# Kernel optimization log

Measured on AMD Instinct MI355X. Metric: run time of the kernel, lower is better.

## Reference

```python
import jax, jax.numpy as jnp
import numpy as np

TEMPERATURE = 0.07
B, D, NUM_CLASSES = 8192, 256, 100

def setup_inputs() -> dict:
    key = jax.random.key(0)
    kz, kl = jax.random.split(key)
    z = jax.random.normal(kz, (B, D), dtype=jnp.float32)
    z = z / jnp.linalg.norm(z, axis=-1, keepdims=True)  # unit-norm embeddings keep exp(logits/T) finite
    labels = jax.random.randint(kl, (B,), 0, NUM_CLASSES, dtype=jnp.int64)
    return {"z": z, "labels": labels}

def reference(z, labels):
    n = z.shape[0]
    same = labels[:, None] == labels[None, :]              # [B, B] bool
    eye = jnp.eye(n, dtype=bool)
    pos_mask = (same & ~eye).astype(z.dtype)               # positives exclude self
    neg_mask = (~same).astype(z.dtype)                     # mask == 0 entries
    exp_logits = jnp.exp(z @ z.T / TEMPERATURE)            # [B, B]
    sum_neg = jnp.sum(exp_logits * neg_mask, axis=1)       # [B]
    # per positive pair: -log(e_ij / (e_ij + sum_neg_i))
    pair_loss = jnp.log1p(sum_neg[:, None] / exp_logits)   # = -log(e/(e+sn)), stable form
    pos_cnt = jnp.sum(pos_mask, axis=1)                    # [B]
    row_loss = jnp.sum(pair_loss * pos_mask, axis=1) / jnp.maximum(pos_cnt, 1.0)
    valid = (pos_cnt > 0).astype(z.dtype)
    n_valid = jnp.sum(valid)
    loss = jnp.where(n_valid > 0,
                     jnp.sum(row_loss * valid) / jnp.maximum(n_valid, 1.0),
                     jnp.zeros((), z.dtype))
    return loss
```

## Files before the change

kernel.cpp:

```cpp
#include <hip/hip_runtime.h>
#include <hip/hip_bf16.h>


#define BN 8192
#define DD 256
#define INV_T (1.0f / 0.07f)
#define CAPI 256
#define CAP 160
#define IPAD 164

typedef __attribute__((ext_vector_type(8))) __bf16 bf16x8;
typedef __attribute__((ext_vector_type(4))) float f32x4;

static __device__ __forceinline__ unsigned short f2bf(float f) {
    unsigned int u = __builtin_bit_cast(unsigned int, f);
    u = (u + 0x7FFFu + ((u >> 16) & 1u)) >> 16;
    return (unsigned short)u;
}
static __device__ __forceinline__ float bf2f(unsigned short s) {
    unsigned int u = (unsigned int)s << 16;
    return __builtin_bit_cast(float, u);
}

__global__ __launch_bounds__(256) void k_prep(const float* __restrict__ z,
                                              unsigned short* __restrict__ zbf2,
                                              const int* __restrict__ labels,
                                              int* __restrict__ cls_cnt,
                                              int* __restrict__ cls_idx) {
    const int gid = blockIdx.x * 256 + threadIdx.x;
    const float4* z4 = (const float4*)z;
    float4 v0 = z4[gid * 2 + 0];
    float4 v1 = z4[gid * 2 + 1];
    unsigned short r[8];
    r[0] = f2bf(v0.x); r[1] = f2bf(v0.y); r[2] = f2bf(v0.z); r[3] = f2bf(v0.w);
    r[4] = f2bf(v1.x); r[5] = f2bf(v1.y); r[6] = f2bf(v1.z); r[7] = f2bf(v1.w);
    const int j = gid >> 5, c5 = gid & 31;
    const int idx16 = (((j >> 4) * 8 + (c5 >> 2)) * 64) + (c5 & 3) * 16 + (j & 15);
    ((uint4*)zbf2)[idx16] = *(const uint4*)r;
    if (gid < BN) {
        const int c = labels[gid];
        const int slot = atomicAdd(&cls_cnt[c], 1);
        if (slot < CAPI) cls_idx[c * CAPI + slot] = gid;
    }
}

__global__ __launch_bounds__(512, 2) void k_passA(const char* __restrict__ zb2,
                                                  float* __restrict__ sn_part) {
    __shared__ float sn_lds[64];
    const int tid = threadIdx.x;
    const int w = tid >> 6, lane = tid & 63;
    const int l15 = lane & 15, lk = lane >> 4;
    const int rowbase = (blockIdx.x >> 2) * 64;
    const int cq = blockIdx.x & 3;
    const int jt0 = cq * 128 + w * 16;

    if (tid < 64) sn_lds[tid] = 0.f;
    __syncthreads();

    const int rt0 = rowbase >> 4;
    bf16x8 a[4][8];
#pragma unroll
    for (int m = 0; m < 4; ++m) {
        const char* p = zb2 + ((size_t)(rt0 + m) * 8192) + lane * 16;
#pragma unroll
        for (int kf = 0; kf < 8; ++kf)
            a[m][kf] = *(const bf16x8*)(p + kf * 1024);
    }

    float snp[4][4] = {};
    bf16x8 b0[8], b1[8];

    auto loadB = [&](bf16x8 (&dst)[8], int jt) {
        const char* p = zb2 + ((size_t)jt * 8192) + lane * 16;
#pragma unroll
        for (int kf = 0; kf < 8; ++kf)
            dst[kf] = *(const bf16x8*)(p + kf * 1024);
    };
    auto computeTile = [&](bf16x8 (&bx)[8], int jt) {
        f32x4 acc[4] = {};
        __builtin_amdgcn_s_setprio(1);
#pragma unroll
        for (int kf = 0; kf < 8; ++kf)
#pragma unroll
            for (int m = 0; m < 4; ++m)
                acc[m] = __builtin_amdgcn_mfma_f32_16x16x32_bf16(a[m][kf], bx[kf], acc[m], 0, 0, 0);
        __builtin_amdgcn_s_setprio(0);
        const int jj = jt * 16 + l15;
#pragma unroll
        for (int m = 0; m < 4; ++m) {
            const int ig = rowbase + m * 16 + lk * 4;
#pragma unroll
            for (int rr = 0; rr < 4; ++rr) {
                float e = __expf(acc[m][rr] * INV_T);
                if (ig + rr == jj) e = 0.f;
                snp[m][rr] += e;
            }
        }
    };

    loadB(b0, jt0);
    for (int t = 0; t < 16; t += 2) {
        loadB(b1, jt0 + t + 1);
        computeTile(b0, jt0 + t);
        if (t + 2 < 16) loadB(b0, jt0 + t + 2);
        computeTile(b1, jt0 + t + 1);
    }

#pragma unroll
    for (int m = 0; m < 4; ++m) {
#pragma unroll
        for (int rr = 0; rr < 4; ++rr) {
            float v = snp[m][rr];
            v += __shfl_xor(v, 1, 64);
            v += __shfl_xor(v, 2, 64);
            v += __shfl_xor(v, 4, 64);
            v += __shfl_xor(v, 8, 64);
            if (l15 == 0)
                atomicAdd(&sn_lds[m * 16 + lk * 4 + rr], v);
        }
    }
    __syncthreads();
    if (tid < 64)
        sn_part[(size_t)cq * BN + rowbase + tid] = sn_lds[tid];
}

__global__ __launch_bounds__(512) void k_passB(const float* __restrict__ zf,
                                               const float* __restrict__ sn_part,
                                               const int* __restrict__ cls_cnt,
                                               const int* __restrict__ cls_idx,
                                               float* __restrict__ gacc) {
    __shared__ char Zc[CAP * 512];
    __shared__ unsigned short dmat[CAP * IPAD];
    __shared__ int glist[CAP];
    __shared__ float snl[CAP];
    __shared__ float sums[CAP];
    __shared__ float blkL;

    const int c = blockIdx.x;
    const int tid = threadIdx.x;
    const int w = tid >> 6, lane = tid & 63;
    const int l15 = lane & 15, lk = lane >> 4;

    const int n_c = min(cls_cnt[c], CAP);
    const int nt = (n_c + 15) >> 4;
    const int rows_p = nt * 16;

    if (tid < CAP) glist[tid] = (tid < n_c) ? cls_idx[c * CAPI + tid] : 0;
    if (tid == 0) blkL = 0.f;
    __syncthreads();

    for (int e2 = w * 2; e2 < rows_p; e2 += 16) {
        const int row = e2 + (lane >> 5);
        const int li = lane & 31;
        const float* src = zf + (size_t)glist[row] * DD + li * 8;
        float4 v0 = *(const float4*)(src);
        float4 v1 = *(const float4*)(src + 4);
        unsigned short r[8];
        r[0] = f2bf(v0.x); r[1] = f2bf(v0.y); r[2] = f2bf(v0.z); r[3] = f2bf(v0.w);
        r[4] = f2bf(v1.x); r[5] = f2bf(v1.y); r[6] = f2bf(v1.z); r[7] = f2bf(v1.w);
        *(uint4*)(Zc + row * 512 + ((li * 16) ^ ((row & 7) << 4))) = *(const uint4*)r;
    }
    __syncthreads();

    for (int mi = w; mi < nt; mi += 8) {
        const int rowA = mi * 16 + l15;
        const int swa = (rowA & 7) << 4;
        bf16x8 a[8];
#pragma unroll
        for (int kf = 0; kf < 8; ++kf)
            a[kf] = *(const bf16x8*)(Zc + rowA * 512 + ((lk * 16 + kf * 64) ^ swa));
        float sp[4] = {};
        for (int nj = 0; nj < nt; ++nj) {
            const int colB = nj * 16 + l15;
            const int swb = (colB & 7) << 4;
            bf16x8 b[8];
#pragma unroll
            for (int kf = 0; kf < 8; ++kf)
                b[kf] = *(const bf16x8*)(Zc + colB * 512 + ((lk * 16 + kf * 64) ^ swb));
            f32x4 acc = {};
#pragma unroll
            for (int kf = 0; kf < 8; ++kf)
                acc = __builtin_amdgcn_mfma_f32_16x16x32_bf16(a[kf], b[kf], acc, 0, 0, 0);
            unsigned short ep[4];
#pragma unroll
            for (int rr = 0; rr < 4; ++rr) {
                const int i = mi * 16 + lk * 4 + rr;
                const float e = __expf(acc[rr] * INV_T);
                ep[rr] = f2bf(e);
                sp[rr] += (colB < n_c && i != colB) ? e : 0.f;
            }
            uint2 uv;
            uv.x = (unsigned)ep[0] | ((unsigned)ep[1] << 16);
            uv.y = (unsigned)ep[2] | ((unsigned)ep[3] << 16);
            *(uint2*)&dmat[colB * IPAD + mi * 16 + lk * 4] = uv;
        }
#pragma unroll
        for (int rr = 0; rr < 4; ++rr) {
            float v = sp[rr];
            v += __shfl_xor(v, 1, 64);
            v += __shfl_xor(v, 2, 64);
            v += __shfl_xor(v, 4, 64);
            v += __shfl_xor(v, 8, 64);
            if (l15 == 0) sums[mi * 16 + lk * 4 + rr] = v;
        }
    }
    __syncthreads();
    if (tid < CAP)
        snl[tid] = (tid < n_c)
            ? (sn_part[glist[tid]] + sn_part[BN + glist[tid]]
               + sn_part[2 * BN + glist[tid]] + sn_part[3 * BN + glist[tid]]
               - sums[tid])
            : 0.f;
    __syncthreads();

    for (int mi = w; mi < nt; mi += 8) {
        float sneg[4];
#pragma unroll
        for (int rr = 0; rr < 4; ++rr) {
            const int i = mi * 16 + lk * 4 + rr;
            sneg[rr] = (i < n_c) ? snl[i] : 0.f;
        }
        float sp[4] = {};
        for (int nj = 0; nj < nt; ++nj) {
            const int colB = nj * 16 + l15;
            const uint2 pk = *(const uint2*)&dmat[colB * IPAD + mi * 16 + lk * 4];
            float ev[4];
            ev[0] = bf2f((unsigned short)(pk.x & 0xffff));
            ev[1] = bf2f((unsigned short)(pk.x >> 16));
            ev[2] = bf2f((unsigned short)(pk.y & 0xffff));
            ev[3] = bf2f((unsigned short)(pk.y >> 16));
#pragma unroll
            for (int rr = 0; rr < 4; ++rr) {
                const int i = mi * 16 + lk * 4 + rr;
                const float t = log1pf(sneg[rr] / ev[rr]);
                sp[rr] += (colB < n_c && i != colB) ? t : 0.f;
            }
        }
#pragma unroll
        for (int rr = 0; rr < 4; ++rr) {
            float v = sp[rr];
            v += __shfl_xor(v, 1, 64);
            v += __shfl_xor(v, 2, 64);
            v += __shfl_xor(v, 4, 64);
            v += __shfl_xor(v, 8, 64);
            const int i = mi * 16 + lk * 4 + rr;
            if (l15 == 0 && i < n_c && n_c > 1)
                atomicAdd(&blkL, v / (float)(n_c - 1));
        }
    }
    __syncthreads();
    if (tid == 0 && n_c > 1) {
        atomicAdd(&gacc[0], blkL);
        atomicAdd(&gacc[1], (float)n_c);
    }
}

__global__ void k_final(const float* __restrict__ gacc, float* __restrict__ out) {
    if (threadIdx.x == 0) {
        const float L = gacc[0], V = gacc[1];
        out[0] = (V > 0.f) ? L / fmaxf(V, 1.f) : 0.f;
    }
}

extern "C" void kernel_launch(void* const* d_in, const int* in_sizes, int n_in,
                              void* d_out, int out_size, void* d_ws, size_t ws_size,
                              hipStream_t stream) {
    const float* z      = (const float*)d_in[0];
    const int*   labels = (const int*)d_in[1];
    float* out = (float*)d_out;

    char* ws = (char*)d_ws;
    unsigned short* zbf2 = (unsigned short*)ws;
    size_t off = (size_t)BN * DD * sizeof(unsigned short);
    float* sn_part = (float*)(ws + off);  off += 4 * BN * sizeof(float);
    int*   cls_cnt = (int*)(ws + off);    off += 1024;
    float* gacc    = (float*)(ws + off);  off += 8;
    int*   cls_idx = (int*)(ws + off);    off += 100 * CAPI * sizeof(int);

    hipMemsetAsync(cls_cnt, 0, 1032, stream);
    k_prep  <<<1024, 256, 0, stream>>>(z, zbf2, labels, cls_cnt, cls_idx);
    k_passA <<<512, 512, 0, stream>>>((const char*)zbf2, sn_part);
    k_passB <<<100, 512, 0, stream>>>(z, sn_part, cls_cnt, cls_idx, gacc);
    k_final <<<1, 64, 0, stream>>>(gacc, out);
}
```

Before: 87.74 us.

## Retile negative-sum pass, drop diagonal masking, split class pass across two blocks

The negative-sum pass now uses 256-thread blocks. Each wave owns 8 row tiles (128 rows) over a 16-column-tile chunk, which raises A-fragment reuse and cuts B loads per MFMA. Per-row sums go straight into one global array through atomics, replacing the LDS reduction and the 4-way partial buffer. The diagonal masks are removed from both passes because the self term cancels when the in-class sum is subtracted. The class pass is launched with a second grid dimension so each class's row tiles are split across two blocks, doubling parallelism at the cost of loading the class embeddings twice. The larger register footprint (64 A fragments plus accumulators) risks spills or lower occupancy.

```diff
diff --git a/kernel.cpp b/kernel.cpp
--- a/kernel.cpp
+++ b/kernel.cpp
@@ -44,30 +44,27 @@
     }
 }
 
-__global__ __launch_bounds__(512, 2) void k_passA(const char* __restrict__ zb2,
-                                                  float* __restrict__ sn_part) {
-    __shared__ float sn_lds[64];
+__global__ __launch_bounds__(256, 2) void k_passA(const char* __restrict__ zb2,
+                                                  float* __restrict__ sn) {
     const int tid = threadIdx.x;
     const int w = tid >> 6, lane = tid & 63;
     const int l15 = lane & 15, lk = lane >> 4;
-    const int rowbase = (blockIdx.x >> 2) * 64;
-    const int cq = blockIdx.x & 3;
-    const int jt0 = cq * 128 + w * 16;
-
-    if (tid < 64) sn_lds[tid] = 0.f;
-    __syncthreads();
-
-    const int rt0 = rowbase >> 4;
-    bf16x8 a[4][8];
-#pragma unroll
-    for (int m = 0; m < 4; ++m) {
+    const int rowblk = blockIdx.x >> 5;
+    const int cchunk = blockIdx.x & 31;
+    const int rowwave = rowblk * 512 + w * 128;
+    const int jt0 = cchunk * 16;
+
+    const int rt0 = rowwave >> 4;
+    bf16x8 a[8][8];
+#pragma unroll
+    for (int m = 0; m < 8; ++m) {
         const char* p = zb2 + ((size_t)(rt0 + m) * 8192) + lane * 16;
 #pragma unroll
         for (int kf = 0; kf < 8; ++kf)
             a[m][kf] = *(const bf16x8*)(p + kf * 1024);
     }
 
-    float snp[4][4] = {};
+    float snp[8][4] = {};
     bf16x8 b0[8], b1[8];
 
     auto loadB = [&](bf16x8 (&dst)[8], int jt) {
@@ -76,38 +73,32 @@
         for (int kf = 0; kf < 8; ++kf)
             dst[kf] = *(const bf16x8*)(p + kf * 1024);
     };
-    auto computeTile = [&](bf16x8 (&bx)[8], int jt) {
-        f32x4 acc[4] = {};
-        __builtin_amdgcn_s_setprio(1);
-#pragma unroll
-        for (int kf = 0; kf < 8; ++kf)
-#pragma unroll
-            for (int m = 0; m < 4; ++m)
+    auto computeTile = [&](bf16x8 (&bx)[8]) {
+        f32x4 acc[8];
+#pragma unroll
+        for (int m = 0; m < 8; ++m) acc[m] = (f32x4){0.f, 0.f, 0.f, 0.f};
+#pragma unroll
+        for (int kf = 0; kf < 8; ++kf)
+#pragma unroll
+            for (int m = 0; m < 8; ++m)
                 acc[m] = __builtin_amdgcn_mfma_f32_16x16x32_bf16(a[m][kf], bx[kf], acc[m], 0, 0, 0);
-        __builtin_amdgcn_s_setprio(0);
-        const int jj = jt * 16 + l15;
-#pragma unroll
-        for (int m = 0; m < 4; ++m) {
-            const int ig = rowbase + m * 16 + lk * 4;
-#pragma unroll
-            for (int rr = 0; rr < 4; ++rr) {
-                float e = __expf(acc[m][rr] * INV_T);
-                if (ig + rr == jj) e = 0.f;
-                snp[m][rr] += e;
-            }
-        }
+#pragma unroll
+        for (int m = 0; m < 8; ++m)
+#pragma unroll
+            for (int rr = 0; rr < 4; ++rr)
+                snp[m][rr] += __expf(acc[m][rr] * INV_T);
     };
 
     loadB(b0, jt0);
     for (int t = 0; t < 16; t += 2) {
         loadB(b1, jt0 + t + 1);
-        computeTile(b0, jt0 + t);
+        computeTile(b0);
         if (t + 2 < 16) loadB(b0, jt0 + t + 2);
-        computeTile(b1, jt0 + t + 1);
-    }
-
-#pragma unroll
-    for (int m = 0; m < 4; ++m) {
+        computeTile(b1);
+    }
+
+#pragma unroll
+    for (int m = 0; m < 8; ++m) {
 #pragma unroll
         for (int rr = 0; rr < 4; ++rr) {
             float v = snp[m][rr];
@@ -116,16 +107,13 @@
             v += __shfl_xor(v, 4, 64);
             v += __shfl_xor(v, 8, 64);
             if (l15 == 0)
-                atomicAdd(&sn_lds[m * 16 + lk * 4 + rr], v);
-        }
-    }
-    __syncthreads();
-    if (tid < 64)
-        sn_part[(size_t)cq * BN + rowbase + tid] = sn_lds[tid];
+                atomicAdd(&sn[rowwave + m * 16 + lk * 4 + rr], v);
+        }
+    }
 }
 
 __global__ __launch_bounds__(512) void k_passB(const float* __restrict__ zf,
-                                               const float* __restrict__ sn_part,
+                                               const float* __restrict__ sn,
                                                const int* __restrict__ cls_cnt,
                                                const int* __restrict__ cls_idx,
                                                float* __restrict__ gacc) {
@@ -137,6 +125,7 @@
     __shared__ float blkL;
 
     const int c = blockIdx.x;
+    const int y = blockIdx.y;
     const int tid = threadIdx.x;
     const int w = tid >> 6, lane = tid & 63;
     const int l15 = lane & 15, lk = lane >> 4;
@@ -162,7 +151,7 @@
     }
     __syncthreads();
 
-    for (int mi = w; mi < nt; mi += 8) {
+    for (int mi = 2 * w + y; mi < nt; mi += 16) {
         const int rowA = mi * 16 + l15;
         const int swa = (rowA & 7) << 4;
         bf16x8 a[8];
@@ -184,10 +173,9 @@
             unsigned short ep[4];
 #pragma unroll
             for (int rr = 0; rr < 4; ++rr) {
-                const int i = mi * 16 + lk * 4 + rr;
                 const float e = __expf(acc[rr] * INV_T);
                 ep[rr] = f2bf(e);
-                sp[rr] += (colB < n_c && i != colB) ? e : 0.f;
+                sp[rr] += (colB < n_c) ? e : 0.f;
             }
             uint2 uv;
             uv.x = (unsigned)ep[0] | ((unsigned)ep[1] << 16);
@@ -206,14 +194,10 @@
     }
     __syncthreads();
     if (tid < CAP)
-        snl[tid] = (tid < n_c)
-            ? (sn_part[glist[tid]] + sn_part[BN + glist[tid]]
-               + sn_part[2 * BN + glist[tid]] + sn_part[3 * BN + glist[tid]]
-               - sums[tid])
-            : 0.f;
-    __syncthreads();
-
-    for (int mi = w; mi < nt; mi += 8) {
+        snl[tid] = (tid < n_c) ? (sn[glist[tid]] - sums[tid]) : 0.f;
+    __syncthreads();
+
+    for (int mi = 2 * w + y; mi < nt; mi += 16) {
         float sneg[4];
 #pragma unroll
         for (int rr = 0; rr < 4; ++rr) {
@@ -251,7 +235,7 @@
     __syncthreads();
     if (tid == 0 && n_c > 1) {
         atomicAdd(&gacc[0], blkL);
-        atomicAdd(&gacc[1], (float)n_c);
+        if (y == 0) atomicAdd(&gacc[1], (float)n_c);
     }
 }
 
@@ -272,14 +256,14 @@
     char* ws = (char*)d_ws;
     unsigned short* zbf2 = (unsigned short*)ws;
     size_t off = (size_t)BN * DD * sizeof(unsigned short);
-    float* sn_part = (float*)(ws + off);  off += 4 * BN * sizeof(float);
+    float* sn      = (float*)(ws + off);  off += BN * sizeof(float);
     int*   cls_cnt = (int*)(ws + off);    off += 1024;
     float* gacc    = (float*)(ws + off);  off += 8;
     int*   cls_idx = (int*)(ws + off);    off += 100 * CAPI * sizeof(int);
 
-    hipMemsetAsync(cls_cnt, 0, 1032, stream);
+    hipMemsetAsync(sn, 0, BN * sizeof(float) + 1024 + 8, stream);
     k_prep  <<<1024, 256, 0, stream>>>(z, zbf2, labels, cls_cnt, cls_idx);
-    k_passA <<<512, 512, 0, stream>>>((const char*)zbf2, sn_part);
-    k_passB <<<100, 512, 0, stream>>>(z, sn_part, cls_cnt, cls_idx, gacc);
+    k_passA <<<512, 256, 0, stream>>>((const char*)zbf2, sn);
+    k_passB <<<dim3(100, 2), 512, 0, stream>>>(z, sn, cls_cnt, cls_idx, gacc);
     k_final <<<1, 64, 0, stream>>>(gacc, out);
 }
```

Result: slower. 268.1 us (+205.6%).

## Split per-class pass into gather and two wide grids; atomics for row sums

Applied to the files above, without the earlier changes.

Replaces the single 100-block per-class kernel, which held the class tile and exp matrix in LDS, with three kernels. A gather kernel writes bf16 class rows to global memory, passB1 computes and stores the exp matrix and in-class sums over a 100x10 grid, and passB2 computes the log terms over a 100x10 grid. This spreads the positive-pair work across many more workgroups instead of one block per class. passA now atomically adds into a single sn array instead of writing four partials, and exp is computed as exp2 with a prescaled constant. The cost is extra launches, global round-trips for the gathered rows and exp matrix, and global atomics.

```diff
diff --git a/kernel.cpp b/kernel.cpp
--- a/kernel.cpp
+++ b/kernel.cpp
@@ -4,10 +4,9 @@
 
 #define BN 8192
 #define DD 256
-#define INV_T (1.0f / 0.07f)
+#define K2E 20.609929155556628f
 #define CAPI 256
 #define CAP 160
-#define IPAD 164
 
 typedef __attribute__((ext_vector_type(8))) __bf16 bf16x8;
 typedef __attribute__((ext_vector_type(4))) float f32x4;
@@ -44,9 +43,86 @@
     }
 }
 
+__global__ __launch_bounds__(512) void k_gather(const float* __restrict__ zf,
+                                                const int* __restrict__ cls_cnt,
+                                                const int* __restrict__ cls_idx,
+                                                unsigned short* __restrict__ zcls) {
+    const int c = blockIdx.x;
+    const int w = threadIdx.x >> 6, lane = threadIdx.x & 63;
+    const int n_c = min(cls_cnt[c], CAP);
+    const int rows_p = ((n_c + 15) >> 4) << 4;
+    for (int row = w; row < rows_p; row += 8) {
+        unsigned int pk = 0;
+        if (row < n_c) {
+            const int g = cls_idx[c * CAPI + row];
+            const float2 v = *(const float2*)(zf + (size_t)g * DD + lane * 2);
+            pk = (unsigned)f2bf(v.x) | ((unsigned)f2bf(v.y) << 16);
+        }
+        *(unsigned int*)((char*)zcls + ((size_t)(c * CAP + row)) * 512 + lane * 4) = pk;
+    }
+}
+
+__global__ __launch_bounds__(256) void k_passB1(const unsigned short* __restrict__ zcls,
+                                                const int* __restrict__ cls_cnt,
+                                                unsigned short* __restrict__ emat,
+                                                float* __restrict__ sums_g) {
+    __shared__ float s16[16];
+    const int c = blockIdx.x, t = blockIdx.y;
+    const int n_c = min(cls_cnt[c], CAP);
+    const int nt = (n_c + 15) >> 4;
+    if (t >= nt) return;
+    const int w = threadIdx.x >> 6, lane = threadIdx.x & 63;
+    const int l15 = lane & 15, lk = lane >> 4;
+    const char* zc = (const char*)zcls + (size_t)c * CAP * 512;
+
+    if (threadIdx.x < 16) s16[threadIdx.x] = 0.f;
+    __syncthreads();
+
+    bf16x8 a[8];
+    const char* ap = zc + (size_t)(t * 16 + l15) * 512 + lk * 16;
+#pragma unroll
+    for (int kf = 0; kf < 8; ++kf) a[kf] = *(const bf16x8*)(ap + kf * 64);
+
+    float sp[4] = {};
+    for (int nj = w; nj < nt; nj += 4) {
+        const int colB = nj * 16 + l15;
+        const char* bp = zc + (size_t)colB * 512 + lk * 16;
+        bf16x8 b[8];
+#pragma unroll
+        for (int kf = 0; kf < 8; ++kf) b[kf] = *(const bf16x8*)(bp + kf * 64);
+        f32x4 acc = {};
+#pragma unroll
+        for (int kf = 0; kf < 8; ++kf)
+            acc = __builtin_amdgcn_mfma_f32_16x16x32_bf16(a[kf], b[kf], acc, 0, 0, 0);
+        unsigned short ep[4];
+#pragma unroll
+        for (int rr = 0; rr < 4; ++rr) {
+            const int i = t * 16 + lk * 4 + rr;
+            const float e = exp2f(acc[rr] * K2E);
+            ep[rr] = f2bf(e);
+            sp[rr] += (colB < n_c && i != colB) ? e : 0.f;
+        }
+        uint2 uv;
+        uv.x = (unsigned)ep[0] | ((unsigned)ep[1] << 16);
+        uv.y = (unsigned)ep[2] | ((unsigned)ep[3] << 16);
+        *(uint2*)&emat[((size_t)(c * CAP + colB)) * CAP + t * 16 + lk * 4] = uv;
+    }
+#pragma unroll
+    for (int rr = 0; rr < 4; ++rr) {
+        float v = sp[rr];
+        v += __shfl_xor(v, 1, 64);
+        v += __shfl_xor(v, 2, 64);
+        v += __shfl_xor(v, 4, 64);
+        v += __shfl_xor(v, 8, 64);
+        if (l15 == 0) atomicAdd(&s16[lk * 4 + rr], v);
+    }
+    __syncthreads();
+    if (threadIdx.x < 16)
+        atomicAdd(&sums_g[c * CAP + t * 16 + threadIdx.x], s16[threadIdx.x]);
+}
+
 __global__ __launch_bounds__(512, 2) void k_passA(const char* __restrict__ zb2,
-                                                  float* __restrict__ sn_part) {
-    __shared__ float sn_lds[64];
+                                                  float* __restrict__ sn) {
     const int tid = threadIdx.x;
     const int w = tid >> 6, lane = tid & 63;
     const int l15 = lane & 15, lk = lane >> 4;
@@ -54,9 +130,6 @@
     const int cq = blockIdx.x & 3;
     const int jt0 = cq * 128 + w * 16;
 
-    if (tid < 64) sn_lds[tid] = 0.f;
-    __syncthreads();
-
     const int rt0 = rowbase >> 4;
     bf16x8 a[4][8];
 #pragma unroll
@@ -91,7 +164,7 @@
             const int ig = rowbase + m * 16 + lk * 4;
 #pragma unroll
             for (int rr = 0; rr < 4; ++rr) {
-                float e = __expf(acc[m][rr] * INV_T);
+                float e = exp2f(acc[m][rr] * K2E);
                 if (ig + rr == jj) e = 0.f;
                 snp[m][rr] += e;
             }
@@ -116,142 +189,76 @@
             v += __shfl_xor(v, 4, 64);
             v += __shfl_xor(v, 8, 64);
             if (l15 == 0)
-                atomicAdd(&sn_lds[m * 16 + lk * 4 + rr], v);
-        }
-    }
-    __syncthreads();
-    if (tid < 64)
-        sn_part[(size_t)cq * BN + rowbase + tid] = sn_lds[tid];
-}
-
-__global__ __launch_bounds__(512) void k_passB(const float* __restrict__ zf,
-                                               const float* __restrict__ sn_part,
-                                               const int* __restrict__ cls_cnt,
-                                               const int* __restrict__ cls_idx,
-                                               float* __restrict__ gacc) {
-    __shared__ char Zc[CAP * 512];
-    __shared__ unsigned short dmat[CAP * IPAD];
-    __shared__ int glist[CAP];
-    __shared__ float snl[CAP];
-    __shared__ float sums[CAP];
-    __shared__ float blkL;
-
-    const int c = blockIdx.x;
-    const int tid = threadIdx.x;
-    const int w = tid >> 6, lane = tid & 63;
-    const int l15 = lane & 15, lk = lane >> 4;
-
+                atomicAdd(&sn[rowbase + m * 16 + lk * 4 + rr], v);
+        }
+    }
+}
+
+__global__ __launch_bounds__(256) void k_passB2(const float* __restrict__ sn,
+                                                const float* __restrict__ sums_g,
+                                                const int* __restrict__ cls_cnt,
+                                                const int* __restrict__ cls_idx,
+                                                const unsigned short* __restrict__ emat,
+                                                float* __restrict__ gacc) {
+    __shared__ float snl16[16];
+    __shared__ float ls16[16];
+    const int c = blockIdx.x, t = blockIdx.y;
     const int n_c = min(cls_cnt[c], CAP);
     const int nt = (n_c + 15) >> 4;
-    const int rows_p = nt * 16;
-
-    if (tid < CAP) glist[tid] = (tid < n_c) ? cls_idx[c * CAPI + tid] : 0;
-    if (tid == 0) blkL = 0.f;
-    __syncthreads();
-
-    for (int e2 = w * 2; e2 < rows_p; e2 += 16) {
-        const int row = e2 + (lane >> 5);
-        const int li = lane & 31;
-        const float* src = zf + (size_t)glist[row] * DD + li * 8;
-        float4 v0 = *(const float4*)(src);
-        float4 v1 = *(const float4*)(src + 4);
-        unsigned short r[8];
-        r[0] = f2bf(v0.x); r[1] = f2bf(v0.y); r[2] = f2bf(v0.z); r[3] = f2bf(v0.w);
-        r[4] = f2bf(v1.x); r[5] = f2bf(v1.y); r[6] = f2bf(v1.z); r[7] = f2bf(v1.w);
-        *(uint4*)(Zc + row * 512 + ((li * 16) ^ ((row & 7) << 4))) = *(const uint4*)r;
-    }
-    __syncthreads();
-
-    for (int mi = w; mi < nt; mi += 8) {
-        const int rowA = mi * 16 + l15;
-        const int swa = (rowA & 7) << 4;
-        bf16x8 a[8];
-#pragma unroll
-        for (int kf = 0; kf < 8; ++kf)
-            a[kf] = *(const bf16x8*)(Zc + rowA * 512 + ((lk * 16 + kf * 64) ^ swa));
-        float sp[4] = {};
-        for (int nj = 0; nj < nt; ++nj) {
-            const int colB = nj * 16 + l15;
-            const int swb = (colB & 7) << 4;
-            bf16x8 b[8];
-#pragma unroll
-            for (int kf = 0; kf < 8; ++kf)
-                b[kf] = *(const bf16x8*)(Zc + colB * 512 + ((lk * 16 + kf * 64) ^ swb));
-            f32x4 acc = {};
-#pragma unroll
-            for (int kf = 0; kf < 8; ++kf)
-                acc = __builtin_amdgcn_mfma_f32_16x16x32_bf16(a[kf], b[kf], acc, 0, 0, 0);
-            unsigned short ep[4];
-#pragma unroll
-            for (int rr = 0; rr < 4; ++rr) {
-                const int i = mi * 16 + lk * 4 + rr;
-                const float e = __expf(acc[rr] * INV_T);
-                ep[rr] = f2bf(e);
-                sp[rr] += (colB < n_c && i != colB) ? e : 0.f;
-            }
-            uint2 uv;
-            uv.x = (unsigned)ep[0] | ((unsigned)ep[1] << 16);
-            uv.y = (unsigned)ep[2] | ((unsigned)ep[3] << 16);
-            *(uint2*)&dmat[colB * IPAD + mi * 16 + lk * 4] = uv;
-        }
+    if (t >= nt || n_c <= 1) return;
+    const int w = threadIdx.x >> 6, lane = threadIdx.x & 63;
+    const int l15 = lane & 15, lk = lane >> 4;
+
+    if (threadIdx.x < 16) {
+        const int i = t * 16 + threadIdx.x;
+        float v = 0.f;
+        if (i < n_c) {
+            const int g = cls_idx[c * CAPI + i];
+            v = sn[g] - sums_g[c * CAP + i];
+        }
+        snl16[threadIdx.x] = v;
+        ls16[threadIdx.x] = 0.f;
+    }
+    __syncthreads();
+
+    float sneg[4];
+#pragma unroll
+    for (int rr = 0; rr < 4; ++rr) sneg[rr] = snl16[lk * 4 + rr];
+
+    float sp[4] = {};
+    for (int nj = w; nj < nt; nj += 4) {
+        const int colB = nj * 16 + l15;
+        const uint2 pk = *(const uint2*)&emat[((size_t)(c * CAP + colB)) * CAP + t * 16 + lk * 4];
+        float ev[4];
+        ev[0] = bf2f((unsigned short)(pk.x & 0xffff));
+        ev[1] = bf2f((unsigned short)(pk.x >> 16));
+        ev[2] = bf2f((unsigned short)(pk.y & 0xffff));
+        ev[3] = bf2f((unsigned short)(pk.y >> 16));
 #pragma unroll
         for (int rr = 0; rr < 4; ++rr) {
-            float v = sp[rr];
-            v += __shfl_xor(v, 1, 64);
-            v += __shfl_xor(v, 2, 64);
-            v += __shfl_xor(v, 4, 64);
-            v += __shfl_xor(v, 8, 64);
-            if (l15 == 0) sums[mi * 16 + lk * 4 + rr] = v;
-        }
-    }
-    __syncthreads();
-    if (tid < CAP)
-        snl[tid] = (tid < n_c)
-            ? (sn_part[glist[tid]] + sn_part[BN + glist[tid]]
-               + sn_part[2 * BN + glist[tid]] + sn_part[3 * BN + glist[tid]]
-               - sums[tid])
-            : 0.f;
-    __syncthreads();
-
-    for (int mi = w; mi < nt; mi += 8) {
-        float sneg[4];
-#pragma unroll
-        for (int rr = 0; rr < 4; ++rr) {
-            const int i = mi * 16 + lk * 4 + rr;
-            sneg[rr] = (i < n_c) ? snl[i] : 0.f;
-        }
-        float sp[4] = {};
-        for (int nj = 0; nj < nt; ++nj) {
-            const int colB = nj * 16 + l15;
-            const uint2 pk = *(const uint2*)&dmat[colB * IPAD + mi * 16 + lk * 4];
-            float ev[4];
-            ev[0] = bf2f((unsigned short)(pk.x & 0xffff));
-            ev[1] = bf2f((unsigned short)(pk.x >> 16));
-            ev[2] = bf2f((unsigned short)(pk.y & 0xffff));
-            ev[3] = bf2f((unsigned short)(pk.y >> 16));
-#pragma unroll
-            for (int rr = 0; rr < 4; ++rr) {
-                const int i = mi * 16 + lk * 4 + rr;
-                const float t = log1pf(sneg[rr] / ev[rr]);
-                sp[rr] += (colB < n_c && i != colB) ? t : 0.f;
-            }
-        }
-#pragma unroll
-        for (int rr = 0; rr < 4; ++rr) {
-            float v = sp[rr];
-            v += __shfl_xor(v, 1, 64);
-            v += __shfl_xor(v, 2, 64);
-            v += __shfl_xor(v, 4, 64);
-            v += __shfl_xor(v, 8, 64);
-            const int i = mi * 16 + lk * 4 + rr;
-            if (l15 == 0 && i < n_c && n_c > 1)
-                atomicAdd(&blkL, v / (float)(n_c - 1));
-        }
-    }
-    __syncthreads();
-    if (tid == 0 && n_c > 1) {
-        atomicAdd(&gacc[0], blkL);
-        atomicAdd(&gacc[1], (float)n_c);
+            const int i = t * 16 + lk * 4 + rr;
+            const float tl = log1pf(sneg[rr] / ev[rr]);
+            sp[rr] += (colB < n_c && i != colB) ? tl : 0.f;
+        }
+    }
+#pragma unroll
+    for (int rr = 0; rr < 4; ++rr) {
+        float v = sp[rr];
+        v += __shfl_xor(v, 1, 64);
+        v += __shfl_xor(v, 2, 64);
+        v += __shfl_xor(v, 4, 64);
+        v += __shfl_xor(v, 8, 64);
+        if (l15 == 0) {
+            const int i = t * 16 + lk * 4 + rr;
+            if (i < n_c) atomicAdd(&ls16[lk * 4 + rr], v);
+        }
+    }
+    __syncthreads();
+    if (threadIdx.x == 0) {
+        float L = 0.f;
+        for (int i = 0; i < 16; ++i) L += ls16[i];
+        atomicAdd(&gacc[0], L / (float)(n_c - 1));
+        if (t == 0) atomicAdd(&gacc[1], (float)n_c);
     }
 }
 
@@ -272,14 +279,21 @@
     char* ws = (char*)d_ws;
     unsigned short* zbf2 = (unsigned short*)ws;
     size_t off = (size_t)BN * DD * sizeof(unsigned short);
-    float* sn_part = (float*)(ws + off);  off += 4 * BN * sizeof(float);
+    char* mz = ws + off;
+    float* sn      = (float*)(ws + off);  off += BN * sizeof(float);
     int*   cls_cnt = (int*)(ws + off);    off += 1024;
-    float* gacc    = (float*)(ws + off);  off += 8;
+    float* gacc    = (float*)(ws + off);  off += 256;
+    float* sums_g  = (float*)(ws + off);  off += 100 * CAP * sizeof(float);
+    size_t mz_bytes = (size_t)((ws + off) - mz);
     int*   cls_idx = (int*)(ws + off);    off += 100 * CAPI * sizeof(int);
-
-    hipMemsetAsync(cls_cnt, 0, 1032, stream);
+    unsigned short* zcls = (unsigned short*)(ws + off); off += (size_t)100 * CAP * DD * 2;
+    unsigned short* emat = (unsigned short*)(ws + off); off += (size_t)100 * CAP * CAP * 2;
+
+    hipMemsetAsync(mz, 0, mz_bytes, stream);
     k_prep  <<<1024, 256, 0, stream>>>(z, zbf2, labels, cls_cnt, cls_idx);
-    k_passA <<<512, 512, 0, stream>>>((const char*)zbf2, sn_part);
-    k_passB <<<100, 512, 0, stream>>>(z, sn_part, cls_cnt, cls_idx, gacc);
+    k_gather<<<100, 512, 0, stream>>>(z, cls_cnt, cls_idx, zcls);
+    k_passB1<<<dim3(100, 10), 256, 0, stream>>>(zcls, cls_cnt, emat, sums_g);
+    k_passA <<<512, 512, 0, stream>>>((const char*)zbf2, sn);
+    k_passB2<<<dim3(100, 10), 256, 0, stream>>>(sn, sums_g, cls_cnt, cls_idx, emat, gacc);
     k_final <<<1, 64, 0, stream>>>(gacc, out);
 }
```

Result: slower. 103.5 us (+18.0%).
